# Kernel optimization log

Measured on AMD Instinct MI355X. Metric: run time of the kernel, lower is better.

The kernel has to match this reference:

```python
import jax, jax.numpy as jnp
import numpy as np


def _sage_mean_layer(x, src, dst, W_self, W_neigh, b):
    # DGL SAGEConv('mean'): h_neigh = mean_{u in N(v)} x_u ; out = x@W_self + h_neigh@W_neigh + b
    n = x.shape[0]
    msg_sum = jax.ops.segment_sum(x[src], dst, num_segments=n)          # [N, D] scatter-add
    deg = jax.ops.segment_sum(jnp.ones_like(dst, dtype=x.dtype), dst, num_segments=n)
    h_neigh = msg_sum / jnp.maximum(deg, 1.0)[:, None]                   # zero-degree nodes -> 0
    return x @ W_self + h_neigh @ W_neigh + b


def setup_inputs() -> dict:
    key = jax.random.key(0)
    ks = jax.random.split(key, 9)
    N, E, D_in, D_hid, D_out = 50000, 800000, 128, 128, 128
    s = lambda d: 1.0 / np.sqrt(d)
    return {
        "x": jax.random.normal(ks[0], (N, D_in), dtype=jnp.float32),
        "src": jax.random.randint(ks[1], (E,), 0, N, dtype=jnp.int32),
        "dst": jax.random.randint(ks[2], (E,), 0, N, dtype=jnp.int32),
        "W1_self": jax.random.uniform(ks[3], (D_in, D_hid), jnp.float32, -s(D_in), s(D_in)),
        "W1_neigh": jax.random.uniform(ks[4], (D_in, D_hid), jnp.float32, -s(D_in), s(D_in)),
        "b1": jnp.zeros((D_hid,), jnp.float32),
        "W2_self": jax.random.uniform(ks[5], (D_hid, D_out), jnp.float32, -s(D_hid), s(D_hid)),
        "W2_neigh": jax.random.uniform(ks[6], (D_hid, D_out), jnp.float32, -s(D_hid), s(D_hid)),
        "b2": jnp.zeros((D_out,), jnp.float32),
    }


def reference(x, src, dst, W1_self, W1_neigh, b1, W2_self, W2_neigh, b2):
    # layer 1: SAGEConv -> ELU (dropout is identity in eval mode)
    h = jax.nn.elu(_sage_mean_layer(x, src, dst, W1_self, W1_neigh, b1))
    # layer 2: is_out_layer=True -> no activation
    return _sage_mean_layer(h, src, dst, W2_self, W2_neigh, b2)
```

## Files before the change

### kernel.cpp

```cpp
#include <hip/hip_runtime.h>
#include <hip/hip_bf16.h>
#include <math.h>

#define DD 128
#define CAP 64
#define LDSP 136

typedef __attribute__((ext_vector_type(8))) short short8;
typedef __attribute__((ext_vector_type(4))) float floatx4;
typedef __attribute__((ext_vector_type(8))) unsigned short ushortx8;

static __device__ __forceinline__ unsigned pack2bf(float a, float b) {
    __hip_bfloat16 ba = __float2bfloat16(a), bb = __float2bfloat16(b);
    return (unsigned)*(ushort*)&ba | ((unsigned)*(ushort*)&bb << 16);
}

#define BF2F(u) __uint_as_float((unsigned)(u) << 16)

__global__ __launch_bounds__(256) void prep_kernel(
        const float* __restrict__ x,
        const int* __restrict__ src, const int* __restrict__ dst,
        int* __restrict__ cnt, int* __restrict__ slot,
        const float* __restrict__ W1a, const float* __restrict__ W1b,
        const float* __restrict__ W2a, const float* __restrict__ W2b,
        ushort* __restrict__ Wp1, ushort* __restrict__ Wp2,
        ushort* __restrict__ Xb,
        int E, int n8, int fill_blocks, int cast_blocks) {
    int b = blockIdx.x;
    if (b < fill_blocks) {
        int e = b * 256 + threadIdx.x;
        if (e < E) {
            int d = dst[e];
            int s = src[e];
            int p = atomicAdd(&cnt[d], 1);
            if (p < CAP) slot[(size_t)d * CAP + p] = s;
        }
    } else if (b < fill_blocks + cast_blocks) {
        int i = (b - fill_blocks) * 256 + threadIdx.x;
        if (i < n8) {
            const float4* xp = (const float4*)x;
            float4 v0 = xp[(size_t)i * 2];
            float4 v1 = xp[(size_t)i * 2 + 1];
            uint4 o;
            o.x = pack2bf(v0.x, v0.y);
            o.y = pack2bf(v0.z, v0.w);
            o.z = pack2bf(v1.x, v1.y);
            o.w = pack2bf(v1.z, v1.w);
            *(uint4*)&Xb[(size_t)i * 8] = o;
        }
    } else {
        int gid = (b - fill_blocks - cast_blocks) * 256 + threadIdx.x;
        int layer = gid >> 15;
        int r = gid & 32767;
        int j = r & 7;
        int lane = (r >> 3) & 63;
        int nt = (r >> 9) & 7;
        int ks = r >> 12;
        int k = ks * 32 + (lane >> 4) * 8 + j;
        int col = nt * 16 + (lane & 15);
        const float* W = layer ? (k < 128 ? W2a : W2b) : (k < 128 ? W1a : W1b);
        float v = W[(k & 127) * DD + col];
        __hip_bfloat16 bf = __float2bfloat16(v);
        (layer ? Wp2 : Wp1)[r] = *(ushort*)&bf;
    }
}

__global__ __launch_bounds__(256) void sage_layer_kernel(
        const ushort* __restrict__ Xin, const int* __restrict__ cnt,
        const int* __restrict__ slot, const ushort* __restrict__ Wp,
        const float* __restrict__ bias,
        ushort* __restrict__ out_bf16, float* __restrict__ out_f32,
        int n, int do_elu) {
    __shared__ ushort hn[16 * LDSP];

    const int row0 = blockIdx.x * 16;
    const int w    = threadIdx.x >> 6;
    const int lane = threadIdx.x & 63;
    const int g  = lane >> 4;
    const int sl = lane & 15;
    const int c  = sl * 8;

    int dv[4], idxv[4];
#pragma unroll
    for (int t = 0; t < 4; ++t) {
        int v = row0 + w * 4 + t;
        dv[t] = (v < n) ? cnt[v] : 0;
    }
#pragma unroll
    for (int t = 0; t < 4; ++t) {
        int d = dv[t] > CAP ? CAP : dv[t];
        dv[t] = d;
        int v = row0 + w * 4 + t;
        int li = lane < d ? lane : (d - 1);
        idxv[t] = (d > 0) ? slot[(size_t)v * CAP + li] : 0;
    }

#pragma unroll
    for (int t = 0; t < 4; ++t) {
        const int d = dv[t];
        const int idx = idxv[t];
        float acc[8];
#pragma unroll
        for (int j = 0; j < 8; ++j) acc[j] = 0.f;

        if (d > 0) {
            int i = 0;
            for (; i + 16 <= d; i += 16) {
                int u0 = __shfl(idx, i + 0 + g);
                int u1 = __shfl(idx, i + 4 + g);
                int u2 = __shfl(idx, i + 8 + g);
                int u3 = __shfl(idx, i + 12 + g);
                ushortx8 y0 = *(const ushortx8*)&Xin[(size_t)u0 * DD + c];
                ushortx8 y1 = *(const ushortx8*)&Xin[(size_t)u1 * DD + c];
                ushortx8 y2 = *(const ushortx8*)&Xin[(size_t)u2 * DD + c];
                ushortx8 y3 = *(const ushortx8*)&Xin[(size_t)u3 * DD + c];
#pragma unroll
                for (int j = 0; j < 8; ++j)
                    acc[j] += BF2F((ushort)y0[j]) + BF2F((ushort)y1[j])
                            + BF2F((ushort)y2[j]) + BF2F((ushort)y3[j]);
            }
            for (; i < d; i += 4) {
                int srcl = i + g;
                int valid = srcl < d;
                int u = __shfl(idx, valid ? srcl : (d - 1));
                float wgt = valid ? 1.f : 0.f;
                ushortx8 y = *(const ushortx8*)&Xin[(size_t)u * DD + c];
#pragma unroll
                for (int j = 0; j < 8; ++j) acc[j] += wgt * BF2F((ushort)y[j]);
            }
        }

#pragma unroll
        for (int j = 0; j < 8; ++j) {
            acc[j] += __shfl_xor(acc[j], 16);
            acc[j] += __shfl_xor(acc[j], 32);
        }

        if (g == 0) {
            float inv = 1.0f / (float)(d > 0 ? d : 1);
            ushort tmp[8];
#pragma unroll
            for (int j = 0; j < 8; ++j) {
                __hip_bfloat16 bq = __float2bfloat16(acc[j] * inv);
                tmp[j] = *(ushort*)&bq;
            }
            uint4 ov;
            ov.x = (unsigned)tmp[0] | ((unsigned)tmp[1] << 16);
            ov.y = (unsigned)tmp[2] | ((unsigned)tmp[3] << 16);
            ov.z = (unsigned)tmp[4] | ((unsigned)tmp[5] << 16);
            ov.w = (unsigned)tmp[6] | ((unsigned)tmp[7] << 16);
            *(uint4*)&hn[(w * 4 + t) * LDSP + c] = ov;
        }
    }

    __syncthreads();

    const int m = lane & 15;
    const int quad = lane >> 4;
    int mrow = row0 + m; if (mrow >= n) mrow = n - 1;
    const ushort* xrow = Xin + (size_t)mrow * DD + quad * 8;
    const ushort* hrow = &hn[m * LDSP + quad * 8];

    floatx4 acc0 = (floatx4){0.f, 0.f, 0.f, 0.f};
    floatx4 acc1 = (floatx4){0.f, 0.f, 0.f, 0.f};

#pragma unroll
    for (int ks = 0; ks < 8; ++ks) {
        short8 a = (ks < 4) ? *(const short8*)(xrow + ks * 32)
                            : *(const short8*)(hrow + (ks - 4) * 32);
        const ushort* wp = Wp + ((size_t)(ks * 8) * 64 + lane) * 8;
        short8 b0 = *(const short8*)(wp + (size_t)(w * 2 + 0) * 64 * 8);
        short8 b1 = *(const short8*)(wp + (size_t)(w * 2 + 1) * 64 * 8);
        acc0 = __builtin_amdgcn_mfma_f32_16x16x32_bf16(a, b0, acc0, 0, 0, 0);
        acc1 = __builtin_amdgcn_mfma_f32_16x16x32_bf16(a, b1, acc1, 0, 0, 0);
    }

#pragma unroll
    for (int q = 0; q < 2; ++q) {
        int nt = w * 2 + q;
        int col = nt * 16 + m;
        float bv = bias[col];
        floatx4 av = q ? acc1 : acc0;
#pragma unroll
        for (int r = 0; r < 4; ++r) {
            int row = row0 + quad * 4 + r;
            if (row >= n) continue;
            float vv = av[r] + bv;
            if (do_elu) vv = vv > 0.f ? vv : expm1f(vv);
            if (out_f32) {
                out_f32[(size_t)row * DD + col] = vv;
            } else {
                __hip_bfloat16 bq = __float2bfloat16(vv);
                out_bf16[(size_t)row * DD + col] = *(ushort*)&bq;
            }
        }
    }
}


extern "C" void kernel_launch(void* const* d_in, const int* in_sizes, int n_in,
                              void* d_out, int out_size, void* d_ws, size_t ws_size,
                              hipStream_t stream) {
    const float* x   = (const float*)d_in[0];
    const int*   src = (const int*)d_in[1];
    const int*   dst = (const int*)d_in[2];
    const float* W1s = (const float*)d_in[3];
    const float* W1n = (const float*)d_in[4];
    const float* b1  = (const float*)d_in[5];
    const float* W2s = (const float*)d_in[6];
    const float* W2n = (const float*)d_in[7];
    const float* b2  = (const float*)d_in[8];
    float* out = (float*)d_out;

    const int N = in_sizes[0] / DD;
    const int E = in_sizes[1];

    char* ws = (char*)d_ws;
    int* cnt       = (int*)ws; ws += (size_t)N * 4;
    int* slot      = (int*)ws; ws += (size_t)N * CAP * 4;
    ushort* Wp1    = (ushort*)ws; ws += 65536;
    ushort* Wp2    = (ushort*)ws; ws += 65536;
    ushort* Xb     = (ushort*)ws; ws += (size_t)N * DD * 2;
    ushort* H1     = (ushort*)ws; ws += (size_t)N * DD * 2;

    (void)hipMemsetAsync(cnt, 0, (size_t)N * 4, stream);

    const int fill_blocks = (E + 255) / 256;
    const int n8 = N * DD / 8;
    const int cast_blocks = (n8 + 255) / 256;
    prep_kernel<<<fill_blocks + cast_blocks + 256, 256, 0, stream>>>(
        x, src, dst, cnt, slot, W1s, W1n, W2s, W2n, Wp1, Wp2, Xb,
        E, n8, fill_blocks, cast_blocks);

    const int nstrips = (N + 15) / 16;

    sage_layer_kernel<<<nstrips, 256, 0, stream>>>(Xb, cnt, slot, Wp1, b1, H1, nullptr, N, 1);
    sage_layer_kernel<<<nstrips, 256, 0, stream>>>(H1, cnt, slot, Wp2, b2, nullptr, out, N, 0);
}
```

Baseline: 243.9 us.

## Shard CSR fill by destination range and unify neighbor gather loop

The edge-bucketing fill now uses a fixed grid of blocks, each assigned one of 8 destination shards. Every block strides over all edges but only performs atomics and slot writes for destinations inside its shard, which is meant to localize atomic and slot-write traffic to a smaller address range per block. The cost is that every shard re-reads the full dst array, so dst is read 8 times. Separately, the neighbor-gather loop merges the 16-wide main loop and the remainder loop into a single masked 4-load loop, which removes the tail path but wastes loads on padded slots.

```diff
diff --git a/kernel.cpp b/kernel.cpp
--- a/kernel.cpp
+++ b/kernel.cpp
@@ -5,6 +5,9 @@
 #define DD 128
 #define CAP 64
 #define LDSP 136
+#define NSHARD 8
+#define FILL_BLOCKS 4096
+#define PACK_BLOCKS 256
 
 typedef __attribute__((ext_vector_type(8))) short short8;
 typedef __attribute__((ext_vector_type(4))) float floatx4;
@@ -14,7 +17,6 @@
     __hip_bfloat16 ba = __float2bfloat16(a), bb = __float2bfloat16(b);
     return (unsigned)*(ushort*)&ba | ((unsigned)*(ushort*)&bb << 16);
 }
-
 #define BF2F(u) __uint_as_float((unsigned)(u) << 16)
 
 __global__ __launch_bounds__(256) void prep_kernel(
@@ -25,18 +27,46 @@
         const float* __restrict__ W2a, const float* __restrict__ W2b,
         ushort* __restrict__ Wp1, ushort* __restrict__ Wp2,
         ushort* __restrict__ Xb,
-        int E, int n8, int fill_blocks, int cast_blocks) {
+        int E, int n8, int shard_size, int cast_blocks) {
     int b = blockIdx.x;
-    if (b < fill_blocks) {
-        int e = b * 256 + threadIdx.x;
-        if (e < E) {
+    if (b < FILL_BLOCKS) {
+        int shard = b & (NSHARD - 1);
+        int chunk = b >> 3;
+        int lo = shard * shard_size;
+        int hi = lo + shard_size;
+        const int stride = (FILL_BLOCKS >> 3) * 256;
+        int e = chunk * 256 + threadIdx.x;
+        for (; e + 3 * stride < E; e += 4 * stride) {
+            int d0 = dst[e];
+            int d1 = dst[e + stride];
+            int d2 = dst[e + 2 * stride];
+            int d3 = dst[e + 3 * stride];
+            if (d0 >= lo && d0 < hi) {
+                int p = atomicAdd(&cnt[d0], 1);
+                if (p < CAP) slot[(size_t)d0 * CAP + p] = src[e];
+            }
+            if (d1 >= lo && d1 < hi) {
+                int p = atomicAdd(&cnt[d1], 1);
+                if (p < CAP) slot[(size_t)d1 * CAP + p] = src[e + stride];
+            }
+            if (d2 >= lo && d2 < hi) {
+                int p = atomicAdd(&cnt[d2], 1);
+                if (p < CAP) slot[(size_t)d2 * CAP + p] = src[e + 2 * stride];
+            }
+            if (d3 >= lo && d3 < hi) {
+                int p = atomicAdd(&cnt[d3], 1);
+                if (p < CAP) slot[(size_t)d3 * CAP + p] = src[e + 3 * stride];
+            }
+        }
+        for (; e < E; e += stride) {
             int d = dst[e];
-            int s = src[e];
-            int p = atomicAdd(&cnt[d], 1);
-            if (p < CAP) slot[(size_t)d * CAP + p] = s;
-        }
-    } else if (b < fill_blocks + cast_blocks) {
-        int i = (b - fill_blocks) * 256 + threadIdx.x;
+            if (d >= lo && d < hi) {
+                int p = atomicAdd(&cnt[d], 1);
+                if (p < CAP) slot[(size_t)d * CAP + p] = src[e];
+            }
+        }
+    } else if (b < FILL_BLOCKS + cast_blocks) {
+        int i = (b - FILL_BLOCKS) * 256 + threadIdx.x;
         if (i < n8) {
             const float4* xp = (const float4*)x;
             float4 v0 = xp[(size_t)i * 2];
@@ -49,7 +79,7 @@
             *(uint4*)&Xb[(size_t)i * 8] = o;
         }
     } else {
-        int gid = (b - fill_blocks - cast_blocks) * 256 + threadIdx.x;
+        int gid = (b - FILL_BLOCKS - cast_blocks) * 256 + threadIdx.x;
         int layer = gid >> 15;
         int r = gid & 32767;
         int j = r & 7;
@@ -59,8 +89,7 @@
         int k = ks * 32 + (lane >> 4) * 8 + j;
         int col = nt * 16 + (lane & 15);
         const float* W = layer ? (k < 128 ? W2a : W2b) : (k < 128 ? W1a : W1b);
-        float v = W[(k & 127) * DD + col];
-        __hip_bfloat16 bf = __float2bfloat16(v);
+        __hip_bfloat16 bf = __float2bfloat16(W[(k & 127) * DD + col]);
         (layer ? Wp2 : Wp1)[r] = *(ushort*)&bf;
     }
 }
@@ -84,12 +113,12 @@
 #pragma unroll
     for (int t = 0; t < 4; ++t) {
         int v = row0 + w * 4 + t;
-        dv[t] = (v < n) ? cnt[v] : 0;
+        int d = (v < n) ? cnt[v] : 0;
+        dv[t] = d > CAP ? CAP : d;
     }
 #pragma unroll
     for (int t = 0; t < 4; ++t) {
-        int d = dv[t] > CAP ? CAP : dv[t];
-        dv[t] = d;
+        int d = dv[t];
         int v = row0 + w * 4 + t;
         int li = lane < d ? lane : (d - 1);
         idxv[t] = (d > 0) ? slot[(size_t)v * CAP + li] : 0;
@@ -102,40 +131,31 @@
         float acc[8];
 #pragma unroll
         for (int j = 0; j < 8; ++j) acc[j] = 0.f;
-
-        if (d > 0) {
-            int i = 0;
-            for (; i + 16 <= d; i += 16) {
-                int u0 = __shfl(idx, i + 0 + g);
-                int u1 = __shfl(idx, i + 4 + g);
-                int u2 = __shfl(idx, i + 8 + g);
-                int u3 = __shfl(idx, i + 12 + g);
-                ushortx8 y0 = *(const ushortx8*)&Xin[(size_t)u0 * DD + c];
-                ushortx8 y1 = *(const ushortx8*)&Xin[(size_t)u1 * DD + c];
-                ushortx8 y2 = *(const ushortx8*)&Xin[(size_t)u2 * DD + c];
-                ushortx8 y3 = *(const ushortx8*)&Xin[(size_t)u3 * DD + c];
-#pragma unroll
-                for (int j = 0; j < 8; ++j)
-                    acc[j] += BF2F((ushort)y0[j]) + BF2F((ushort)y1[j])
-                            + BF2F((ushort)y2[j]) + BF2F((ushort)y3[j]);
-            }
-            for (; i < d; i += 4) {
-                int srcl = i + g;
-                int valid = srcl < d;
-                int u = __shfl(idx, valid ? srcl : (d - 1));
-                float wgt = valid ? 1.f : 0.f;
-                ushortx8 y = *(const ushortx8*)&Xin[(size_t)u * DD + c];
-#pragma unroll
-                for (int j = 0; j < 8; ++j) acc[j] += wgt * BF2F((ushort)y[j]);
-            }
-        }
-
+        const int rounds = (d + 15) >> 4;
+        for (int ri = 0; ri < rounds; ++ri) {
+            int s0 = ri * 16 + g, s1 = s0 + 4, s2 = s0 + 8, s3 = s0 + 12;
+            int u0 = __shfl(idx, s0 < d ? s0 : d - 1);
+            int u1 = __shfl(idx, s1 < d ? s1 : d - 1);
+            int u2 = __shfl(idx, s2 < d ? s2 : d - 1);
+            int u3 = __shfl(idx, s3 < d ? s3 : d - 1);
+            float w0 = s0 < d ? 1.f : 0.f;
+            float w1 = s1 < d ? 1.f : 0.f;
+            float w2 = s2 < d ? 1.f : 0.f;
+            float w3 = s3 < d ? 1.f : 0.f;
+            ushortx8 y0 = *(const ushortx8*)&Xin[(size_t)u0 * DD + c];
+            ushortx8 y1 = *(const ushortx8*)&Xin[(size_t)u1 * DD + c];
+            ushortx8 y2 = *(const ushortx8*)&Xin[(size_t)u2 * DD + c];
+            ushortx8 y3 = *(const ushortx8*)&Xin[(size_t)u3 * DD + c];
+#pragma unroll
+            for (int j = 0; j < 8; ++j)
+                acc[j] += w0 * BF2F((ushort)y0[j]) + w1 * BF2F((ushort)y1[j])
+                        + w2 * BF2F((ushort)y2[j]) + w3 * BF2F((ushort)y3[j]);
+        }
 #pragma unroll
         for (int j = 0; j < 8; ++j) {
             acc[j] += __shfl_xor(acc[j], 16);
             acc[j] += __shfl_xor(acc[j], 32);
         }
-
         if (g == 0) {
             float inv = 1.0f / (float)(d > 0 ? d : 1);
             ushort tmp[8];
@@ -163,18 +183,16 @@
 
     floatx4 acc0 = (floatx4){0.f, 0.f, 0.f, 0.f};
     floatx4 acc1 = (floatx4){0.f, 0.f, 0.f, 0.f};
-
 #pragma unroll
     for (int ks = 0; ks < 8; ++ks) {
         short8 a = (ks < 4) ? *(const short8*)(xrow + ks * 32)
                             : *(const short8*)(hrow + (ks - 4) * 32);
         const ushort* wp = Wp + ((size_t)(ks * 8) * 64 + lane) * 8;
-        short8 b0 = *(const short8*)(wp + (size_t)(w * 2 + 0) * 64 * 8);
-        short8 b1 = *(const short8*)(wp + (size_t)(w * 2 + 1) * 64 * 8);
+        short8 b0 = *(const short8*)(wp + (size_t)(w * 2 + 0) * 512);
+        short8 b1 = *(const short8*)(wp + (size_t)(w * 2 + 1) * 512);
         acc0 = __builtin_amdgcn_mfma_f32_16x16x32_bf16(a, b0, acc0, 0, 0, 0);
         acc1 = __builtin_amdgcn_mfma_f32_16x16x32_bf16(a, b1, acc1, 0, 0, 0);
     }
-
 #pragma unroll
     for (int q = 0; q < 2; ++q) {
         int nt = w * 2 + q;
@@ -184,14 +202,15 @@
 #pragma unroll
         for (int r = 0; r < 4; ++r) {
             int row = row0 + quad * 4 + r;
-            if (row >= n) continue;
-            float vv = av[r] + bv;
-            if (do_elu) vv = vv > 0.f ? vv : expm1f(vv);
-            if (out_f32) {
-                out_f32[(size_t)row * DD + col] = vv;
-            } else {
-                __hip_bfloat16 bq = __float2bfloat16(vv);
-                out_bf16[(size_t)row * DD + col] = *(ushort*)&bq;
+            if (row < n) {
+                float vv = av[r] + bv;
+                if (do_elu) vv = vv > 0.f ? vv : expm1f(vv);
+                if (out_f32) {
+                    out_f32[(size_t)row * DD + col] = vv;
+                } else {
+                    __hip_bfloat16 bq = __float2bfloat16(vv);
+                    out_bf16[(size_t)row * DD + col] = *(ushort*)&bq;
+                }
             }
         }
     }
@@ -225,12 +244,12 @@
 
     (void)hipMemsetAsync(cnt, 0, (size_t)N * 4, stream);
 
-    const int fill_blocks = (E + 255) / 256;
+    const int shard_size = (N + NSHARD - 1) / NSHARD;
     const int n8 = N * DD / 8;
     const int cast_blocks = (n8 + 255) / 256;
-    prep_kernel<<<fill_blocks + cast_blocks + 256, 256, 0, stream>>>(
+    prep_kernel<<<FILL_BLOCKS + cast_blocks + PACK_BLOCKS, 256, 0, stream>>>(
         x, src, dst, cnt, slot, W1s, W1n, W2s, W2n, Wp1, Wp2, Xb,
-        E, n8, fill_blocks, cast_blocks);
+        E, n8, shard_size, cast_blocks);
 
     const int nstrips = (N + 15) / 16;
 
```

Result: faster. 227.8 us (-6.6%).
